# Kernel tuning notes

Measured on AMD Instinct MI355X. Metric: run time of the kernel, lower is better.

Reference implementation:

```python
import jax, jax.numpy as jnp
import numpy as np

N_NODES = 100000
N_EDGES = 1600000


def gcn_conv(x, edge_index, W, b):
    """PyG-style GCNConv: self-loops + symmetric normalization + scatter-add."""
    n = x.shape[0]
    src, dst = edge_index[0], edge_index[1]
    loop = jnp.arange(n, dtype=src.dtype)
    src = jnp.concatenate([src, loop])
    dst = jnp.concatenate([dst, loop])
    h = x @ W  # [n, out] transform before propagate (PyG order)
    deg = jax.ops.segment_sum(jnp.ones_like(dst, dtype=h.dtype), dst, num_segments=n)
    dinv = jnp.where(deg > 0, deg ** -0.5, 0.0)
    norm = dinv[src] * dinv[dst]  # [E+n]
    msgs = h[src] * norm[:, None]  # gather + scale (largest intermediate)
    out = jax.ops.segment_sum(msgs, dst, num_segments=n)
    return out + b


def setup_inputs() -> dict:
    key = jax.random.key(0)
    ks = jax.random.split(key, 8)
    edge_attr = jax.random.normal(ks[0], (N_NODES, 5), dtype=jnp.float32)
    edge_index = jax.random.randint(ks[1], (2, N_EDGES), 0, N_NODES, dtype=jnp.int64)
    def lin(k, fan_in, fan_out):
        bound = 1.0 / np.sqrt(fan_in)
        return jax.random.uniform(k, (fan_in, fan_out), jnp.float32, -bound, bound)
    return {
        "edge_attr": edge_attr,
        "edge_index": edge_index,
        "W1": lin(ks[2], 5, 64),
        "b1": jnp.zeros((64,), jnp.float32),
        "W2": lin(ks[3], 64, 32),
        "b2": jnp.zeros((32,), jnp.float32),
        "fcW1": lin(ks[4], 32, 16),
        "fcb1": jnp.zeros((16,), jnp.float32),
        "fcW2": lin(ks[5], 16, 2),
        "fcb2": jnp.zeros((2,), jnp.float32),
    }


def reference(edge_attr, edge_index, W1, b1, W2, b2, fcW1, fcb1, fcW2, fcb2):
    x = jax.nn.relu(gcn_conv(edge_attr, edge_index, W1, b1))
    x = jax.nn.relu(gcn_conv(x, edge_index, W2, b2))
    x = jax.nn.relu(x @ fcW1 + fcb1)
    return x @ fcW2 + fcb2
```

## Files before the change

### kernel.cpp

```cpp
#include <hip/hip_runtime.h>


#define MS_TILE 2048
#define MAXB 512
#define AGG_NODES 32
#define AGG_STAGE 1024
#define PF_T 512
#define PF_EPT 10
#define PF_OV 1024

typedef __attribute__((ext_vector_type(4))) _Float16 half4;
typedef __attribute__((ext_vector_type(8))) _Float16 half8;

__device__ inline int scan256_incl(int v, int lane, int w, int* wsum,
                                   int* total) {
    int incl = v;
#pragma unroll
    for (int d = 1; d < 64; d <<= 1) {
        int up = __shfl_up(incl, d, 64);
        if (lane >= d) incl += up;
    }
    if (lane == 63) wsum[w] = incl;
    __syncthreads();
    int add = 0;
    if (w > 0) add += wsum[0];
    if (w > 1) add += wsum[1];
    if (w > 2) add += wsum[2];
    *total = wsum[0] + wsum[1] + wsum[2] + wsum[3];
    return incl + add;
}

__global__ __launch_bounds__(256) void histA(const int* __restrict__ dst,
                                             int* __restrict__ histG,
                                             int* __restrict__ histT, int E,
                                             int nTilesP) {
    __shared__ int h[MAXB];
    int t = threadIdx.x;
    h[t] = 0;
    h[t + 256] = 0;
    __syncthreads();
    int base = blockIdx.x * MS_TILE;
    int cnt = min(MS_TILE, E - base);
    for (int k = t; k < cnt; k += 256) atomicAdd(&h[dst[base + k] >> 8], 1);
    __syncthreads();
    histG[blockIdx.x * MAXB + t] = h[t];
    histG[blockIdx.x * MAXB + 256 + t] = h[t + 256];
    histT[t * nTilesP + blockIdx.x] = h[t];
    histT[(t + 256) * nTilesP + blockIdx.x] = h[t + 256];
}

__global__ __launch_bounds__(256) void scanTiles(const int* __restrict__ histT,
                                                 int* __restrict__ offsG,
                                                 int* __restrict__ bucketTotal,
                                                 int nTiles, int nTilesP) {
    __shared__ int wsum[4];
    int b = blockIdx.x, t = threadIdx.x;
    int lane = t & 63, w = t >> 6;
    const int* row = histT + (size_t)b * nTilesP;
    int run = 0;
    for (int base = 0; base < nTiles; base += 256) {
        int idx = base + t;
        int v = (idx < nTiles) ? row[idx] : 0;
        int total;
        int incl = scan256_incl(v, lane, w, wsum, &total);
        if (idx < nTiles) offsG[idx * MAXB + b] = incl - v + run;
        run += total;
        __syncthreads();
    }
    if (t == 0) bucketTotal[b] = run;
}

__global__ __launch_bounds__(256) void multisplit2(
    const int* __restrict__ src, const int* __restrict__ dst,
    const int* __restrict__ histG, const int* __restrict__ offsG,
    const int* __restrict__ btot, int* __restrict__ gbaseOut,
    unsigned* __restrict__ binned, int E) {
    __shared__ unsigned stage[MS_TILE];
    __shared__ unsigned short sb[MS_TILE];
    __shared__ int hoff[MAXB + 1];
    __shared__ int hcur[MAXB];
    __shared__ int gb[MAXB];
    __shared__ int wsum[4];
    int t = threadIdx.x;
    int lane = t & 63, w = t >> 6;
    int tile = blockIdx.x;
    int base = tile * MS_TILE;
    int cnt = min(MS_TILE, E - base);

    int b0 = btot[2 * t], b1v = btot[2 * t + 1];
    int s2 = b0 + b1v;
    int tot2;
    int incl2 = scan256_incl(s2, lane, w, wsum, &tot2);
    int ex2 = incl2 - s2;
    gb[2 * t] = ex2 + offsG[tile * MAXB + 2 * t];
    gb[2 * t + 1] = ex2 + b0 + offsG[tile * MAXB + 2 * t + 1];
    if (tile == 0) {
        gbaseOut[2 * t] = ex2;
        gbaseOut[2 * t + 1] = ex2 + b0;
        if (t == 255) gbaseOut[MAXB] = E;
    }
    __syncthreads();

    int a0 = histG[tile * MAXB + 2 * t];
    int a1 = histG[tile * MAXB + 2 * t + 1];
    int s = a0 + a1;
    int tot;
    int incl = scan256_incl(s, lane, w, wsum, &tot);
    int ex = incl - s;
    hoff[2 * t] = ex;
    hoff[2 * t + 1] = ex + a0;
    hcur[2 * t] = ex;
    hcur[2 * t + 1] = ex + a0;
    if (t == 255) hoff[MAXB] = cnt;
    __syncthreads();
    for (int k = t; k < cnt; k += 256) {
        int d = dst[base + k];
        int b = d >> 8;
        int p = atomicAdd(&hcur[b], 1);
        stage[p] = ((unsigned)src[base + k] << 8) | (unsigned)(d & 255);
        sb[p] = (unsigned short)b;
    }
    __syncthreads();
    for (int k = t; k < cnt; k += 256) {
        int b = sb[k];
        binned[gb[b] + (k - hoff[b])] = stage[k];
    }
}

__global__ __launch_bounds__(PF_T) void place_fine2(
    const unsigned* __restrict__ binned, const int* __restrict__ gbase,
    const float* __restrict__ x, int* __restrict__ offs,
    float* __restrict__ dinv, _Float16* __restrict__ y, int* __restrict__ srcs,
    int n) {
    __shared__ int cnt[256];
    __shared__ int baseL[256];
    __shared__ int wsum[8];
    __shared__ unsigned ovW[PF_OV];
    __shared__ int ovR[PF_OV];
    __shared__ int ovN;
    int t = threadIdx.x, b = blockIdx.x;
    int lane = t & 63, w = t >> 6;
    int node0 = b << 8;
    int nn = min(256, n - node0);
    int e0 = gbase[b], e1 = gbase[b + 1];
    if (t < 256) cnt[t] = 0;
    if (t == 0) ovN = 0;
    __syncthreads();

    unsigned wdv[PF_EPT];
    int rk[PF_EPT];
    int nc = 0;
#pragma unroll
    for (int u = 0; u < PF_EPT; ++u) {
        int k = e0 + t + u * PF_T;
        if (k < e1) {
            unsigned wd = binned[k];
            wdv[u] = wd;
            rk[u] = atomicAdd(&cnt[wd & 255u], 1);
            nc = u + 1;
        }
    }
    for (int k = e0 + t + PF_EPT * PF_T; k < e1; k += PF_T) {
        unsigned wd = binned[k];
        int r = atomicAdd(&cnt[wd & 255u], 1);
        int j = atomicAdd(&ovN, 1);
        if (j < PF_OV) { ovW[j] = wd; ovR[j] = r; }
    }
    __syncthreads();

    int c = (t < 256) ? cnt[t] : 0;
    int incl = c;
#pragma unroll
    for (int d = 1; d < 64; d <<= 1) {
        int up = __shfl_up(incl, d, 64);
        if (lane >= d) incl += up;
    }
    if (lane == 63) wsum[w] = incl;
    __syncthreads();
    int add = 0;
    if (w > 0) add += wsum[0];
    if (w > 1) add += wsum[1];
    if (w > 2) add += wsum[2];
    incl += add;
    if (t < 256) {
        int myoff = e0 + incl - c;
        baseL[t] = myoff;
        if (t < nn) {
            int node = node0 + t;
            offs[node] = myoff;
            float di = 1.0f / sqrtf((float)(c + 1));
            dinv[node] = di;
            const float* xr = x + (size_t)node * 5;
            half8 hv;
            hv[0] = (_Float16)(xr[0] * di);
            hv[1] = (_Float16)(xr[1] * di);
            hv[2] = (_Float16)(xr[2] * di);
            hv[3] = (_Float16)(xr[3] * di);
            hv[4] = (_Float16)(xr[4] * di);
            hv[5] = (_Float16)0.f;
            hv[6] = (_Float16)0.f;
            hv[7] = (_Float16)0.f;
            *(half8*)(y + (size_t)node * 8) = hv;
        }
    }
    __syncthreads();

#pragma unroll
    for (int u = 0; u < PF_EPT; ++u) {
        if (u < nc) {
            unsigned wd = wdv[u];
            srcs[baseL[wd & 255u] + rk[u]] = (int)(wd >> 8);
        }
    }
    int no = ovN;
    for (int j = t; j < no; j += PF_T) {
        unsigned wd = ovW[j];
        srcs[baseL[wd & 255u] + ovR[j]] = (int)(wd >> 8);
    }
}

__global__ __launch_bounds__(256) void agg1_t12(
    const _Float16* __restrict__ y, const int* __restrict__ srcs,
    const int* __restrict__ offs, const float* __restrict__ dinv,
    const float* __restrict__ W1, const float* __restrict__ b1,
    const float* __restrict__ W2, _Float16* __restrict__ h2, int n, int E) {
    __shared__ float w1s[320];
    __shared__ float b1s[64];
    __shared__ float w2s[64 * 32];
    __shared__ float o1[32 * 64];
    __shared__ float zs[32 * 6];
    int t = threadIdx.x;
    w1s[t] = W1[t];
    if (t < 64) {
        w1s[t + 256] = W1[t + 256];
        b1s[t] = b1[t];
    }
#pragma unroll
    for (int r = 0; r < 8; ++r) w2s[r * 256 + t] = W2[r * 256 + t];

    int node0 = blockIdx.x * 32;
    int li = t >> 3, e = t & 7;
    int i = node0 + li;
    const half8* yv = (const half8*)y;
    float a0 = 0.f, a1 = 0.f, a2 = 0.f, a3 = 0.f, a4 = 0.f;
    if (i < n) {
        int off = offs[i];
        int cnt = ((i + 1 < n) ? offs[i + 1] : E) - off;
        if (e == 0) {
            half8 v = yv[i];
            a0 = (float)v[0]; a1 = (float)v[1]; a2 = (float)v[2];
            a3 = (float)v[3]; a4 = (float)v[4];
        }
        for (int p = e; p < cnt; p += 8) {
            half8 v = yv[srcs[off + p]];
            a0 += (float)v[0]; a1 += (float)v[1]; a2 += (float)v[2];
            a3 += (float)v[3]; a4 += (float)v[4];
        }
    }
#pragma unroll
    for (int m = 4; m >= 1; m >>= 1) {
        a0 += __shfl_xor(a0, m, 64);
        a1 += __shfl_xor(a1, m, 64);
        a2 += __shfl_xor(a2, m, 64);
        a3 += __shfl_xor(a3, m, 64);
        a4 += __shfl_xor(a4, m, 64);
    }
    if (i < n && e == 0) {
        float di = dinv[i];
        zs[li * 6 + 0] = a0 * di;
        zs[li * 6 + 1] = a1 * di;
        zs[li * 6 + 2] = a2 * di;
        zs[li * 6 + 3] = a3 * di;
        zs[li * 6 + 4] = a4 * di;
        zs[li * 6 + 5] = di;
    }
    __syncthreads();
#pragma unroll
    for (int r = 0; r < 8; ++r) {
        int idx = r * 256 + t;
        int lj = idx >> 6, f = idx & 63;
        if (node0 + lj < n) {
            const float* zr = zs + lj * 6;
            float acc = b1s[f];
#pragma unroll
            for (int k = 0; k < 5; ++k) acc += zr[k] * w1s[k * 64 + f];
            o1[lj * 64 + f] = fmaxf(acc, 0.0f);
        }
    }
    __syncthreads();
#pragma unroll
    for (int r = 0; r < 4; ++r) {
        int idx = r * 256 + t;
        int lj = idx >> 5, g = idx & 31;
        int i2 = node0 + lj;
        if (i2 < n) {
            float acc = 0.f;
#pragma unroll
            for (int k = 0; k < 64; ++k) acc += o1[lj * 64 + k] * w2s[k * 32 + g];
            h2[(size_t)i2 * 32 + g] = (_Float16)(acc * zs[lj * 6 + 5]);
        }
    }
}

__global__ __launch_bounds__(256) void agg2_fc(
    const _Float16* __restrict__ h, const int* __restrict__ srcs,
    const int* __restrict__ offs, const float* __restrict__ dinv,
    const float* __restrict__ b2, const float* __restrict__ fcW1,
    const float* __restrict__ fcb1, const float* __restrict__ fcW2,
    const float* __restrict__ fcb2, float* __restrict__ out, int n, int E) {
    __shared__ int sidx[AGG_STAGE];
    __shared__ float sm[AGG_NODES * 33];
    __shared__ float x3s[AGG_NODES * 16];
    __shared__ float w1s[512];
    __shared__ float w2s[32];
    __shared__ float b1s[16];
    __shared__ float b2s[2];
    __shared__ float bs2[32];
    int t = threadIdx.x;
    w1s[t] = fcW1[t];
    w1s[t + 256] = fcW1[t + 256];
    if (t < 32) { w2s[t] = fcW2[t]; bs2[t] = b2[t]; }
    if (t < 16) b1s[t] = fcb1[t];
    if (t < 2) b2s[t] = fcb2[t];

    int node0 = blockIdx.x * AGG_NODES;
    int li = t >> 3, fq = t & 7;
    int i = node0 + li;
    bool live = (i < n);
    const char* hb = (const char*)h;

    int e0 = offs[node0];
    int eEnd = (node0 + AGG_NODES < n) ? offs[node0 + AGG_NODES] : E;
    int myOff = 0, myCnt = 0;
    float4 acc = {0.f, 0.f, 0.f, 0.f};
    if (live) {
        myOff = offs[i];
        myCnt = ((i + 1 < n) ? offs[i + 1] : E) - myOff;
        half4 sv = *(const half4*)(hb + ((size_t)i << 6) + (fq << 3));
        acc.x = (float)sv.x; acc.y = (float)sv.y;
        acc.z = (float)sv.z; acc.w = (float)sv.w;
    }

    for (int cs = e0; cs < eEnd; cs += AGG_STAGE) {
        int ce = min(cs + AGG_STAGE, eEnd);
        for (int k = cs + t; k < ce; k += 256) sidx[k - cs] = srcs[k] << 6;
        __syncthreads();
        int ps = max(myOff, cs), pe = min(myOff + myCnt, ce);
        int p = ps;
        for (; p + 8 <= pe; p += 8) {
            int o[8];
#pragma unroll
            for (int u = 0; u < 8; ++u) o[u] = sidx[p + u - cs];
            half4 v[8];
#pragma unroll
            for (int u = 0; u < 8; ++u)
                v[u] = *(const half4*)(hb + o[u] + (fq << 3));
#pragma unroll
            for (int u = 0; u < 8; ++u) {
                acc.x += (float)v[u].x; acc.y += (float)v[u].y;
                acc.z += (float)v[u].z; acc.w += (float)v[u].w;
            }
        }
        for (; p + 4 <= pe; p += 4) {
            int o0 = sidx[p - cs], o1 = sidx[p + 1 - cs];
            int o2 = sidx[p + 2 - cs], o3 = sidx[p + 3 - cs];
            half4 v0 = *(const half4*)(hb + o0 + (fq << 3));
            half4 v1 = *(const half4*)(hb + o1 + (fq << 3));
            half4 v2 = *(const half4*)(hb + o2 + (fq << 3));
            half4 v3 = *(const half4*)(hb + o3 + (fq << 3));
            acc.x += (float)v0.x + (float)v1.x + (float)v2.x + (float)v3.x;
            acc.y += (float)v0.y + (float)v1.y + (float)v2.y + (float)v3.y;
            acc.z += (float)v0.z + (float)v1.z + (float)v2.z + (float)v3.z;
            acc.w += (float)v0.w + (float)v1.w + (float)v2.w + (float)v3.w;
        }
        for (; p < pe; ++p) {
            half4 v = *(const half4*)(hb + sidx[p - cs] + (fq << 3));
            acc.x += (float)v.x; acc.y += (float)v.y;
            acc.z += (float)v.z; acc.w += (float)v.w;
        }
        __syncthreads();
    }

    if (live) {
        float di = dinv[i];
        int f0 = fq << 2;
        sm[li * 33 + f0 + 0] = fmaxf(di * acc.x + bs2[f0 + 0], 0.f);
        sm[li * 33 + f0 + 1] = fmaxf(di * acc.y + bs2[f0 + 1], 0.f);
        sm[li * 33 + f0 + 2] = fmaxf(di * acc.z + bs2[f0 + 2], 0.f);
        sm[li * 33 + f0 + 3] = fmaxf(di * acc.w + bs2[f0 + 3], 0.f);
    }
    __syncthreads();
#pragma unroll
    for (int r = 0; r < 2; ++r) {
        int idx = r * 256 + t;
        int lj = idx >> 4, j = idx & 15;
        if (node0 + lj < n) {
            float a = b1s[j];
#pragma unroll
            for (int k = 0; k < 32; ++k) a += sm[lj * 33 + k] * w1s[k * 16 + j];
            x3s[lj * 16 + j] = fmaxf(a, 0.f);
        }
    }
    __syncthreads();
    if (t < 64) {
        int lj = t >> 1, o = t & 1;
        if (node0 + lj < n) {
            float a = b2s[o];
#pragma unroll
            for (int j = 0; j < 16; ++j) a += x3s[lj * 16 + j] * w2s[j * 2 + o];
            out[(size_t)(node0 + lj) * 2 + o] = a;
        }
    }
}

extern "C" void kernel_launch(void* const* d_in, const int* in_sizes, int n_in,
                              void* d_out, int out_size, void* d_ws, size_t ws_size,
                              hipStream_t stream) {
    const float* edge_attr = (const float*)d_in[0];
    const int* edge_index  = (const int*)d_in[1];
    const float* W1   = (const float*)d_in[2];
    const float* b1   = (const float*)d_in[3];
    const float* W2   = (const float*)d_in[4];
    const float* b2   = (const float*)d_in[5];
    const float* fcW1 = (const float*)d_in[6];
    const float* fcb1 = (const float*)d_in[7];
    const float* fcW2 = (const float*)d_in[8];
    const float* fcb2 = (const float*)d_in[9];
    float* out = (float*)d_out;

    int n = in_sizes[0] / 5;
    int E = in_sizes[1] / 2;
    int NBkt = (n + 255) >> 8;
    int nTiles = (E + MS_TILE - 1) / MS_TILE;
    int nTilesP = (nTiles + 63) & ~63;
    const int* src = edge_index;
    const int* dst = edge_index + E;

    char* ws = (char*)d_ws;
    auto alloc = [&](size_t bytes) {
        char* p = ws;
        ws += (bytes + 255) & ~(size_t)255;
        return p;
    };
    int*      offs   = (int*)alloc((size_t)n * 4);
    float*    dinv   = (float*)alloc((size_t)n * 4);
    int*      histG  = (int*)alloc((size_t)nTiles * MAXB * 4);
    int*      histT  = (int*)alloc((size_t)MAXB * nTilesP * 4);
    int*      offsG  = (int*)alloc((size_t)nTiles * MAXB * 4);
    int*      btot   = (int*)alloc((size_t)MAXB * 4);
    int*      gbase  = (int*)alloc((size_t)(MAXB + 1) * 4);
    int*      srcs   = (int*)alloc((size_t)E * 4);
    unsigned* binned = (unsigned*)alloc((size_t)E * 4);
    _Float16* y      = (_Float16*)alloc((size_t)n * 8 * 2);
    _Float16* h2     = (_Float16*)alloc((size_t)n * 32 * 2);

    histA<<<nTiles, 256, 0, stream>>>(dst, histG, histT, E, nTilesP);
    scanTiles<<<MAXB, 256, 0, stream>>>(histT, offsG, btot, nTiles, nTilesP);
    multisplit2<<<nTiles, 256, 0, stream>>>(src, dst, histG, offsG, btot, gbase,
                                            binned, E);
    place_fine2<<<NBkt, PF_T, 0, stream>>>(binned, gbase, edge_attr, offs, dinv,
                                           y, srcs, n);
    agg1_t12<<<(n + 31) / 32, 256, 0, stream>>>(y, srcs, offs, dinv, W1, b1, W2,
                                                h2, n, E);
    agg2_fc<<<(n + AGG_NODES - 1) / AGG_NODES, 256, 0, stream>>>(
        h2, srcs, offs, dinv, b2, fcW1, fcb1, fcW2, fcb2, out, n, E);
}
```

Measured before the change: 176.9 us.

## Scan tile histograms in tile-major layout, dropping the transposed histogram copy

histA no longer writes a transposed bucket-major histogram. The per-bucket exclusive scan across tiles now reads the tile-major histG directly: each 512-thread block handles 8 buckets, loads 64-tile chunks, and transposes them through LDS before doing a wave-level scan. This removes the strided scattered writes in histA and the extra buffer, and makes the offset writes coalesced. In exchange the scan runs on only 64 blocks, which leaves less parallelism for a serial loop over tiles.

```diff
diff --git a/kernel.cpp b/kernel.cpp
--- a/kernel.cpp
+++ b/kernel.cpp
@@ -31,9 +31,7 @@
 }
 
 __global__ __launch_bounds__(256) void histA(const int* __restrict__ dst,
-                                             int* __restrict__ histG,
-                                             int* __restrict__ histT, int E,
-                                             int nTilesP) {
+                                             int* __restrict__ histG, int E) {
     __shared__ int h[MAXB];
     int t = threadIdx.x;
     h[t] = 0;
@@ -45,29 +43,38 @@
     __syncthreads();
     histG[blockIdx.x * MAXB + t] = h[t];
     histG[blockIdx.x * MAXB + 256 + t] = h[t + 256];
-    histT[t * nTilesP + blockIdx.x] = h[t];
-    histT[(t + 256) * nTilesP + blockIdx.x] = h[t + 256];
-}
-
-__global__ __launch_bounds__(256) void scanTiles(const int* __restrict__ histT,
-                                                 int* __restrict__ offsG,
-                                                 int* __restrict__ bucketTotal,
-                                                 int nTiles, int nTilesP) {
-    __shared__ int wsum[4];
-    int b = blockIdx.x, t = threadIdx.x;
+}
+
+__global__ __launch_bounds__(512) void scanTilesT(const int* __restrict__ histG,
+                                                  int* __restrict__ offsG,
+                                                  int* __restrict__ bucketTotal,
+                                                  int nTiles) {
+    __shared__ int lds[8][66];
+    int t = threadIdx.x;
     int lane = t & 63, w = t >> 6;
-    const int* row = histT + (size_t)b * nTilesP;
-    int run = 0;
-    for (int base = 0; base < nTiles; base += 256) {
-        int idx = base + t;
-        int v = (idx < nTiles) ? row[idx] : 0;
-        int total;
-        int incl = scan256_incl(v, lane, w, wsum, &total);
-        if (idx < nTiles) offsG[idx * MAXB + b] = incl - v + run;
-        run += total;
+    int rr = t >> 3, bb = t & 7;
+    int B0 = blockIdx.x * 8;
+    int carry = 0;
+    for (int c0 = 0; c0 < nTiles; c0 += 64) {
+        int rows = min(64, nTiles - c0);
+        int v = 0;
+        if (rr < rows) v = histG[(size_t)(c0 + rr) * MAXB + B0 + bb];
+        lds[bb][rr] = v;
         __syncthreads();
-    }
-    if (t == 0) bucketTotal[b] = run;
+        int x = lds[w][lane];
+        int incl = x;
+#pragma unroll
+        for (int d = 1; d < 64; d <<= 1) {
+            int up = __shfl_up(incl, d, 64);
+            if (lane >= d) incl += up;
+        }
+        int total = __shfl(incl, 63, 64);
+        lds[w][lane] = incl - x + carry;
+        carry += total;
+        __syncthreads();
+        if (rr < rows) offsG[(size_t)(c0 + rr) * MAXB + B0 + bb] = lds[bb][rr];
+    }
+    if (lane == 0) bucketTotal[B0 + w] = carry;
 }
 
 __global__ __launch_bounds__(256) void multisplit2(
@@ -432,7 +439,6 @@
     int E = in_sizes[1] / 2;
     int NBkt = (n + 255) >> 8;
     int nTiles = (E + MS_TILE - 1) / MS_TILE;
-    int nTilesP = (nTiles + 63) & ~63;
     const int* src = edge_index;
     const int* dst = edge_index + E;
 
@@ -445,7 +451,6 @@
     int*      offs   = (int*)alloc((size_t)n * 4);
     float*    dinv   = (float*)alloc((size_t)n * 4);
     int*      histG  = (int*)alloc((size_t)nTiles * MAXB * 4);
-    int*      histT  = (int*)alloc((size_t)MAXB * nTilesP * 4);
     int*      offsG  = (int*)alloc((size_t)nTiles * MAXB * 4);
     int*      btot   = (int*)alloc((size_t)MAXB * 4);
     int*      gbase  = (int*)alloc((size_t)(MAXB + 1) * 4);
@@ -454,8 +459,8 @@
     _Float16* y      = (_Float16*)alloc((size_t)n * 8 * 2);
     _Float16* h2     = (_Float16*)alloc((size_t)n * 32 * 2);
 
-    histA<<<nTiles, 256, 0, stream>>>(dst, histG, histT, E, nTilesP);
-    scanTiles<<<MAXB, 256, 0, stream>>>(histT, offsG, btot, nTiles, nTilesP);
+    histA<<<nTiles, 256, 0, stream>>>(dst, histG, E);
+    scanTilesT<<<MAXB / 8, 512, 0, stream>>>(histG, offsG, btot, nTiles);
     multisplit2<<<nTiles, 256, 0, stream>>>(src, dst, histG, offsG, btot, gbase,
                                             binned, E);
     place_fine2<<<NBkt, PF_T, 0, stream>>>(binned, gbase, edge_attr, offs, dinv,
```

Result: no change. 179.5 us (+1.5%).
